# Optimization experiments

Hardware: AMD Instinct MI355X
Metric: run time of the kernel (lower is better)

## Reference

```python
import jax, jax.numpy as jnp
import numpy as np

D_MODEL = 1024
N_HEADS = 16
D_K = D_MODEL // N_HEADS
D_FF = 4096
EPS = 1e-5


def _layernorm(x, g, b):
    mu = jnp.mean(x, axis=-1, keepdims=True)
    var = jnp.mean(jnp.square(x - mu), axis=-1, keepdims=True)
    return (x - mu) * jax.lax.rsqrt(var + EPS) * g + b


def setup_inputs() -> dict:
    key = jax.random.key(0)
    ks = jax.random.split(key, 16)
    s = 0.02
    B, S = 2, 2048
    inp = {
        "x": jax.random.normal(ks[0], (B, S, D_MODEL), dtype=jnp.float32),
        "mask": jnp.ones((1, 1, S, S), dtype=jnp.int32),
        # attention projections (stored [in, out]; y = x @ W + b)
        "Wq": jax.random.normal(ks[1], (D_MODEL, D_MODEL)) * s,
        "bq": jnp.zeros((D_MODEL,)),
        "Wk": jax.random.normal(ks[2], (D_MODEL, D_MODEL)) * s,
        "bk": jnp.zeros((D_MODEL,)),
        "Wv": jax.random.normal(ks[3], (D_MODEL, D_MODEL)) * s,
        "bv": jnp.zeros((D_MODEL,)),
        "Wo": jax.random.normal(ks[4], (D_MODEL, D_MODEL)) * s,
        "bo": jnp.zeros((D_MODEL,)),
        "temperature": jnp.sqrt(jnp.array([float(D_K)], dtype=jnp.float32)),
        "time_weights": jax.random.normal(ks[5], (1, N_HEADS, 1, D_K)),
        "gateW": jax.random.normal(ks[6], (D_K, 1)) * s,
        "gateb": jnp.zeros((1,)),
        "ln_attn_g": jnp.ones((D_MODEL,)),
        "ln_attn_b": jnp.zeros((D_MODEL,)),
        # feed-forward
        "fc1W": jax.random.normal(ks[7], (D_MODEL, D_FF)) * s,
        "fc1b": jnp.zeros((D_FF,)),
        "fc2W": jax.random.normal(ks[8], (D_FF, D_MODEL)) * s,
        "fc2b": jnp.zeros((D_MODEL,)),
        "n1g": jnp.ones((D_MODEL,)),
        "n1b": jnp.zeros((D_MODEL,)),
        "n2g": jnp.ones((D_MODEL,)),
        "n2b": jnp.zeros((D_MODEL,)),
    }
    return inp


def reference(x, mask, Wq, bq, Wk, bk, Wv, bv, Wo, bo, temperature,
              time_weights, gateW, gateb, ln_attn_g, ln_attn_b,
              fc1W, fc1b, fc2W, fc2b, n1g, n1b, n2g, n2b):
    B, S, D = x.shape
    H, dk = N_HEADS, D_K

    def heads(t):  # [B,S,D] -> [B,H,S,dk]
        return t.reshape(B, S, H, dk).transpose(0, 2, 1, 3)

    q = heads(x @ Wq + bq) + time_weights  # learned per-head bias on Q
    k = heads(x @ Wk + bk)
    v = heads(x @ Wv + bv)

    scores = jnp.einsum("bhqd,bhkd->bhqk", q, k) / temperature
    scores = jnp.where(mask == 0, jnp.float32(-1e9), scores)
    gate = jax.nn.sigmoid(q @ gateW + gateb)  # [B,H,S,1] per-query gate
    scores = scores * gate
    probs = jax.nn.softmax(scores, axis=-1)

    ctx = jnp.einsum("bhqk,bhkd->bhqd", probs, v)
    ctx = ctx.transpose(0, 2, 1, 3).reshape(B, S, D)
    attn_out = _layernorm(ctx @ Wo + bo, ln_attn_g, ln_attn_b)

    x1 = _layernorm(x + attn_out, n1g, n1b)
    ff = jax.nn.gelu(x1 @ fc1W + fc1b, approximate=False) @ fc2W + fc2b
    return _layernorm(x1 + ff, n2g, n2b)
```

## Files before the change

### kernel.cpp

```cpp
#include <hip/hip_runtime.h>
#include <stdint.h>
#include <math.h>


typedef uint16_t u16;
typedef unsigned long long u64;
typedef __attribute__((ext_vector_type(8))) short short8;
typedef __attribute__((ext_vector_type(4))) float f32x4;

#define S_LEN 2048
#define DM 1024

#define GLOAD_LDS16(g, l)                                                      \
  __builtin_amdgcn_global_load_lds(                                            \
      (const __attribute__((address_space(1))) void*)(g),                      \
      (__attribute__((address_space(3))) void*)(l), 16, 0, 0)

__device__ __forceinline__ float bf2f(u16 h) {
  union { uint32_t u; float f; } x;
  x.u = ((uint32_t)h) << 16;
  return x.f;
}
__device__ __forceinline__ u16 f2bf(float f) {
  union { float f; uint32_t u; } x;
  x.f = f;
  uint32_t r = (x.u + 0x7fffu + ((x.u >> 16) & 1u)) >> 16;
  return (u16)r;
}
__device__ __forceinline__ u16 f2bf_fast(float f) {
  union { float f; uint32_t u; } x;
  x.f = f;
  return (u16)((x.u + 0x8000u) >> 16);
}

union U8 { uint4 u; u16 s[8]; };
union U4 { uint2 u; u16 s[4]; };

__global__ __launch_bounds__(256) void cvt_k(const float* __restrict__ in,
                                             u16* __restrict__ out, int n) {
  int i = (blockIdx.x * 256 + threadIdx.x) * 4;
  if (i >= n) return;
  float4 v = *(const float4*)(in + i);
  U4 o;
  o.s[0] = f2bf(v.x); o.s[1] = f2bf(v.y); o.s[2] = f2bf(v.z); o.s[3] = f2bf(v.w);
  *(uint2*)(out + i) = o.u;
}

__global__ __launch_bounds__(256) void mb_k(const int* __restrict__ mask,
                                            u16* __restrict__ mb) {
  int tid = blockIdx.x * 256 + threadIdx.x;
  const int* src = mask + (size_t)tid * 16;
  uint32_t b = 0;
#pragma unroll
  for (int q = 0; q < 4; q++) {
    int4 m = *(const int4*)(src + q * 4);
    b |= (m.x != 0 ? 1u : 0u) << (q * 4 + 0);
    b |= (m.y != 0 ? 1u : 0u) << (q * 4 + 1);
    b |= (m.z != 0 ? 1u : 0u) << (q * 4 + 2);
    b |= (m.w != 0 ? 1u : 0u) << (q * 4 + 3);
  }
  mb[tid] = (u16)b;
}

__device__ __forceinline__ void tcvt_body(const float* __restrict__ in,
                                          u16* __restrict__ out, int R, int C) {
  __shared__ u16 tile[64][72];
  int c0 = blockIdx.x * 64, r0 = blockIdx.y * 64;
  int t = threadIdx.x;
  int r = t & 63, seg = t >> 6;
  const float* src = in + (size_t)(r0 + r) * C + c0 + seg * 16;
#pragma unroll
  for (int q = 0; q < 4; q++) {
    float4 v = *(const float4*)(src + q * 4);
    tile[r][seg * 16 + q * 4 + 0] = f2bf(v.x);
    tile[r][seg * 16 + q * 4 + 1] = f2bf(v.y);
    tile[r][seg * 16 + q * 4 + 2] = f2bf(v.z);
    tile[r][seg * 16 + q * 4 + 3] = f2bf(v.w);
  }
  __syncthreads();
  U8 v0, v1;
#pragma unroll
  for (int i = 0; i < 8; i++) v0.s[i] = tile[seg * 16 + i][r];
#pragma unroll
  for (int i = 0; i < 8; i++) v1.s[i] = tile[seg * 16 + 8 + i][r];
  u16* dst = out + (size_t)(c0 + r) * R + r0 + seg * 16;
  *(uint4*)dst = v0.u;
  *(uint4*)(dst + 8) = v1.u;
}

__global__ __launch_bounds__(256) void transpose_cvt_k(const float* __restrict__ in,
                                                       u16* __restrict__ out,
                                                       int R, int C) {
  tcvt_body(in, out, R, C);
}

__global__ __launch_bounds__(256) void transpose_cvt3_k(const float* __restrict__ i0,
                                                        const float* __restrict__ i1,
                                                        const float* __restrict__ i2,
                                                        u16* __restrict__ o0,
                                                        u16* __restrict__ o1,
                                                        u16* __restrict__ o2) {
  int z = blockIdx.z;
  const float* in = (z == 0) ? i0 : (z == 1) ? i1 : i2;
  u16* out = (z == 0) ? o0 : (z == 1) ? o1 : o2;
  tcvt_body(in, out, 1024, 1024);
}

__global__ __launch_bounds__(256) void vtrans_k(const u16* __restrict__ V,
                                                u16* __restrict__ VT) {
  __shared__ u16 tile[64][72];
  int bx = blockIdx.x, bh = blockIdx.y;
  int b = bh >> 4, h = bh & 15;
  int t = threadIdx.x, r = t & 63, seg = t >> 6;
  const u16* src = V + (size_t)(b * S_LEN + bx * 64 + r) * DM + h * 64 + seg * 16;
  *(uint4*)&tile[r][seg * 16] = *(const uint4*)src;
  *(uint4*)&tile[r][seg * 16 + 8] = *(const uint4*)(src + 8);
  __syncthreads();
  U8 v0, v1;
#pragma unroll
  for (int i = 0; i < 8; i++) v0.s[i] = tile[seg * 16 + i][r];
#pragma unroll
  for (int i = 0; i < 8; i++) v1.s[i] = tile[seg * 16 + 8 + i][r];
  u16* dst = VT + ((size_t)bh * 64 + r) * S_LEN + bx * 64 + seg * 16;
  *(uint4*)dst = v0.u;
  *(uint4*)(dst + 8) = v1.u;
}

template <int BM, int EPI, int MXS>
__global__ __launch_bounds__(256) void gemm_bt(const u16* __restrict__ A,
                                               const u16* __restrict__ Bt,
                                               u16* __restrict__ C,
                                               const float* __restrict__ bias,
                                               int M, int N, int K) {
  constexpr int MI = BM / 32;
  constexpr int RPW = BM / 4;
  __shared__ u16 As[BM * 32];
  __shared__ u16 Bs[128 * 32];
  int t = threadIdx.x;
  int wid = t >> 6, lane = t & 63;
  int g = lane >> 4, li = lane & 15;
  int bx = MXS ? blockIdx.y : blockIdx.x;
  int by = MXS ? blockIdx.x : blockIdx.y;
  int wr = (wid >> 1) * (BM / 2), wc = (wid & 1) * 64;

  const u16* a0 = A + (size_t)(by * BM + wid * RPW + (lane >> 2)) * K + (lane & 3) * 8;
  const u16* b0 = Bt + (size_t)(bx * 128 + wid * 32 + (lane >> 2)) * K + (lane & 3) * 8;
  u16* lA0 = &As[wid * RPW * 32];
  u16* lB0 = &Bs[wid * 1024];

  f32x4 acc[MI][4];
#pragma unroll
  for (int i = 0; i < MI; i++)
#pragma unroll
    for (int j = 0; j < 4; j++) acc[i][j] = (f32x4){0.f, 0.f, 0.f, 0.f};

  for (int k0 = 0; k0 < K; k0 += 32) {
    GLOAD_LDS16(a0 + k0, lA0);
    if (BM == 128) GLOAD_LDS16(a0 + (size_t)16 * K + k0, lA0 + 512);
    GLOAD_LDS16(b0 + k0, lB0);
    GLOAD_LDS16(b0 + (size_t)16 * K + k0, lB0 + 512);
    __syncthreads();
    short8 af[MI], bfv[4];
#pragma unroll
    for (int i = 0; i < MI; i++)
      af[i] = *(const short8*)&As[(wr + i * 16 + li) * 32 + g * 8];
#pragma unroll
    for (int i = 0; i < 4; i++)
      bfv[i] = *(const short8*)&Bs[(wc + i * 16 + li) * 32 + g * 8];
#pragma unroll
    for (int mi = 0; mi < MI; mi++)
#pragma unroll
      for (int ni = 0; ni < 4; ni++)
        acc[mi][ni] = __builtin_amdgcn_mfma_f32_16x16x32_bf16(
            af[mi], bfv[ni], acc[mi][ni], 0, 0, 0);
    __syncthreads();
  }

#pragma unroll
  for (int ni = 0; ni < 4; ni++) {
    int col = bx * 128 + wc + ni * 16 + li;
    float bv = bias[col];
#pragma unroll
    for (int mi = 0; mi < MI; mi++) {
#pragma unroll
      for (int r = 0; r < 4; r++) {
        int row = by * BM + wr + mi * 16 + g * 4 + r;
        float v = acc[mi][ni][r] + bv;
        if (EPI == 2) v = 0.5f * v * (1.0f + erff(v * 0.70710678118654752f));
        C[(size_t)row * N + col] = f2bf(v);
      }
    }
  }
}

__global__ __launch_bounds__(256) void qkv_gemm(const u16* __restrict__ A,
                                                const u16* __restrict__ WTq,
                                                const u16* __restrict__ WTk,
                                                const u16* __restrict__ WTv,
                                                u16* __restrict__ Cq,
                                                u16* __restrict__ Ck,
                                                u16* __restrict__ Cv,
                                                const float* __restrict__ bq,
                                                const float* __restrict__ bk,
                                                const float* __restrict__ bv,
                                                const float* __restrict__ tw) {
  const int K = 1024, N = 1024;
  __shared__ u16 As[128 * 32];
  __shared__ u16 Bs[128 * 32];
  int t = threadIdx.x;
  int wid = t >> 6, lane = t & 63;
  int g = lane >> 4, li = lane & 15;
  int by = blockIdx.x, bx = blockIdx.y, z = blockIdx.z;
  int wr = (wid >> 1) * 64, wc = (wid & 1) * 64;

  const u16* Bt = (z == 0) ? WTq : (z == 1) ? WTk : WTv;
  u16* C = (z == 0) ? Cq : (z == 1) ? Ck : Cv;
  const float* bias = (z == 0) ? bq : (z == 1) ? bk : bv;

  const u16* a0 = A + (size_t)(by * 128 + wid * 32 + (lane >> 2)) * K + (lane & 3) * 8;
  const u16* b0 = Bt + (size_t)(bx * 128 + wid * 32 + (lane >> 2)) * K + (lane & 3) * 8;
  u16* lA0 = &As[wid * 1024];
  u16* lB0 = &Bs[wid * 1024];

  f32x4 acc[4][4];
#pragma unroll
  for (int i = 0; i < 4; i++)
#pragma unroll
    for (int j = 0; j < 4; j++) acc[i][j] = (f32x4){0.f, 0.f, 0.f, 0.f};

  for (int k0 = 0; k0 < K; k0 += 32) {
    GLOAD_LDS16(a0 + k0, lA0);
    GLOAD_LDS16(a0 + (size_t)16 * K + k0, lA0 + 512);
    GLOAD_LDS16(b0 + k0, lB0);
    GLOAD_LDS16(b0 + (size_t)16 * K + k0, lB0 + 512);
    __syncthreads();
    short8 af[4], bfv[4];
#pragma unroll
    for (int i = 0; i < 4; i++)
      af[i] = *(const short8*)&As[(wr + i * 16 + li) * 32 + g * 8];
#pragma unroll
    for (int i = 0; i < 4; i++)
      bfv[i] = *(const short8*)&Bs[(wc + i * 16 + li) * 32 + g * 8];
#pragma unroll
    for (int mi = 0; mi < 4; mi++)
#pragma unroll
      for (int ni = 0; ni < 4; ni++)
        acc[mi][ni] = __builtin_amdgcn_mfma_f32_16x16x32_bf16(
            af[mi], bfv[ni], acc[mi][ni], 0, 0, 0);
    __syncthreads();
  }

#pragma unroll
  for (int ni = 0; ni < 4; ni++) {
    int col = bx * 128 + wc + ni * 16 + li;
    float bvv = bias[col];
    if (z == 0) bvv += tw[col];
#pragma unroll
    for (int mi = 0; mi < 4; mi++) {
#pragma unroll
      for (int r = 0; r < 4; r++) {
        int row = by * 128 + wr + mi * 16 + g * 4 + r;
        C[(size_t)row * N + col] = f2bf(acc[mi][ni][r] + bvv);
      }
    }
  }
}

__global__ __launch_bounds__(256) void attn_k(const u16* __restrict__ Q,
                                              const u16* __restrict__ Kp,
                                              const u16* __restrict__ VT,
                                              u16* __restrict__ CTX,
                                              const u16* __restrict__ mb,
                                              const float* __restrict__ gateW,
                                              const float* __restrict__ gateb,
                                              const float* __restrict__ temp) {
  __shared__ u16 Qs[64][72];
  __shared__ u16 Ks[64][72];
  __shared__ u16 Vs[64][72];
  __shared__ u16 Ps[4][16][72];
  __shared__ float gate_s[64];

  int blk = blockIdx.x;
  int bh = blk & 31, qt = blk >> 5;
  int b = bh >> 4, h = bh & 15;
  int t = threadIdx.x, wid = t >> 6, lane = t & 63;
  int g = lane >> 4, li = lane & 15;
  int sq0 = qt * 64;

  const u16* Qb  = Q + ((size_t)b * S_LEN) * DM + h * 64;
  const u16* Kb  = Kp + ((size_t)b * S_LEN) * DM + h * 64;
  const u16* VTb = VT + ((size_t)(b * 16 + h) * 64) * S_LEN;

  {
    int r = t >> 2, cs = (t & 3) * 16;
    const u16* src = Qb + (size_t)(sq0 + r) * DM + cs;
    *(uint4*)&Qs[r][cs] = *(const uint4*)src;
    *(uint4*)&Qs[r][cs + 8] = *(const uint4*)(src + 8);
  }
  __syncthreads();
  if (t < 64) {
    float acc = gateb[0];
#pragma unroll
    for (int d = 0; d < 64; d++) acc += bf2f(Qs[t][d]) * gateW[d];
    gate_s[t] = 1.f / (1.f + __expf(-acc));
  }
  __syncthreads();

  const float LOG2E = 1.4426950408889634f;
  float invt2 = LOG2E / temp[0];
  const float NEG2 = -1.0e9f * 1.4426950408889634f;
  short8 qf0 = *(const short8*)&Qs[wid * 16 + li][g * 8];
  short8 qf1 = *(const short8*)&Qs[wid * 16 + li][32 + g * 8];
  float gqs[4], ng[4];
  int sq[4];
#pragma unroll
  for (int r = 0; r < 4; r++) {
    float gq = gate_s[wid * 16 + g * 4 + r];
    gqs[r] = gq * invt2;
    ng[r] = NEG2 * gq;
    sq[r] = sq0 + wid * 16 + g * 4 + r;
  }

  float m_i[4], psl[4];
  f32x4 o[4];
#pragma unroll
  for (int r = 0; r < 4; r++) { m_i[r] = -1e30f; psl[r] = 0.f; }
#pragma unroll
  for (int n = 0; n < 4; n++) o[n] = (f32x4){0.f, 0.f, 0.f, 0.f};

  for (int kt = 0; kt < 32; kt++) {
    __syncthreads();
    {
      int r = t >> 2, cs = (t & 3) * 16;
      const u16* srcK = Kb + (size_t)(kt * 64 + r) * DM + cs;
      *(uint4*)&Ks[r][cs] = *(const uint4*)srcK;
      *(uint4*)&Ks[r][cs + 8] = *(const uint4*)(srcK + 8);
      const u16* srcV = VTb + (size_t)r * S_LEN + kt * 64 + cs;
      *(uint4*)&Vs[r][cs] = *(const uint4*)srcV;
      *(uint4*)&Vs[r][cs + 8] = *(const uint4*)(srcV + 8);
    }
    u64 bits[4];
#pragma unroll
    for (int r = 0; r < 4; r++)
      bits[r] = *(const u64*)(mb + (size_t)sq[r] * 128 + kt * 4);
    __syncthreads();

    f32x4 sc[4];
#pragma unroll
    for (int ni = 0; ni < 4; ni++) {
      sc[ni] = (f32x4){0.f, 0.f, 0.f, 0.f};
      short8 kf0 = *(const short8*)&Ks[ni * 16 + li][g * 8];
      short8 kf1 = *(const short8*)&Ks[ni * 16 + li][32 + g * 8];
      sc[ni] = __builtin_amdgcn_mfma_f32_16x16x32_bf16(qf0, kf0, sc[ni], 0, 0, 0);
      sc[ni] = __builtin_amdgcn_mfma_f32_16x16x32_bf16(qf1, kf1, sc[ni], 0, 0, 0);
    }

    float sval[4][4];
    float rmax[4] = {-1e30f, -1e30f, -1e30f, -1e30f};
    bool allm = ((bits[0] & bits[1] & bits[2] & bits[3]) == ~0ull);
    if (__all(allm)) {
#pragma unroll
      for (int ni = 0; ni < 4; ni++)
#pragma unroll
        for (int r = 0; r < 4; r++) {
          float s = sc[ni][r] * gqs[r];
          sval[ni][r] = s;
          rmax[r] = fmaxf(rmax[r], s);
        }
    } else {
      u64 bs[4];
#pragma unroll
      for (int r = 0; r < 4; r++) bs[r] = bits[r] >> li;
#pragma unroll
      for (int ni = 0; ni < 4; ni++)
#pragma unroll
        for (int r = 0; r < 4; r++) {
          float s = ((bs[r] >> (ni * 16)) & 1ull) ? sc[ni][r] * gqs[r] : ng[r];
          sval[ni][r] = s;
          rmax[r] = fmaxf(rmax[r], s);
        }
    }
#pragma unroll
    for (int off = 1; off < 16; off <<= 1)
#pragma unroll
      for (int r = 0; r < 4; r++)
        rmax[r] = fmaxf(rmax[r], __shfl_xor(rmax[r], off, 64));

    float alpha[4];
#pragma unroll
    for (int r = 0; r < 4; r++) {
      float mnew = fmaxf(m_i[r], rmax[r]);
      alpha[r] = __builtin_amdgcn_exp2f(m_i[r] - mnew);
      m_i[r] = mnew;
    }
    float pp[4] = {0.f, 0.f, 0.f, 0.f};
#pragma unroll
    for (int ni = 0; ni < 4; ni++)
#pragma unroll
      for (int r = 0; r < 4; r++) {
        float p = __builtin_amdgcn_exp2f(sval[ni][r] - m_i[r]);
        pp[r] += p;
        Ps[wid][g * 4 + r][ni * 16 + li] = f2bf_fast(p);
      }
#pragma unroll
    for (int r = 0; r < 4; r++) psl[r] = psl[r] * alpha[r] + pp[r];
#pragma unroll
    for (int n = 0; n < 4; n++)
#pragma unroll
      for (int r = 0; r < 4; r++) o[n][r] *= alpha[r];

    __builtin_amdgcn_wave_barrier();

    short8 pf0 = *(const short8*)&Ps[wid][li][g * 8];
    short8 pf1 = *(const short8*)&Ps[wid][li][32 + g * 8];
#pragma unroll
    for (int ni = 0; ni < 4; ni++) {
      short8 vf0 = *(const short8*)&Vs[ni * 16 + li][g * 8];
      short8 vf1 = *(const short8*)&Vs[ni * 16 + li][32 + g * 8];
      o[ni] = __builtin_amdgcn_mfma_f32_16x16x32_bf16(pf0, vf0, o[ni], 0, 0, 0);
      o[ni] = __builtin_amdgcn_mfma_f32_16x16x32_bf16(pf1, vf1, o[ni], 0, 0, 0);
    }
  }

  float linv[4];
#pragma unroll
  for (int r = 0; r < 4; r++) {
    float l = psl[r];
#pragma unroll
    for (int off = 1; off < 16; off <<= 1) l += __shfl_xor(l, off, 64);
    linv[r] = 1.f / l;
  }
#pragma unroll
  for (int ni = 0; ni < 4; ni++) {
    int col = h * 64 + ni * 16 + li;
#pragma unroll
    for (int r = 0; r < 4; r++) {
      size_t row = (size_t)b * S_LEN + sq[r];
      CTX[row * DM + col] = f2bf(o[ni][r] * linv[r]);
    }
  }
}

__device__ __forceinline__ void block_sum2(float& a, float& b, float* red, int t) {
#pragma unroll
  for (int off = 32; off > 0; off >>= 1) {
    a += __shfl_xor(a, off, 64);
    b += __shfl_xor(b, off, 64);
  }
  __syncthreads();
  if ((t & 63) == 0) {
    red[(t >> 6) * 2] = a;
    red[(t >> 6) * 2 + 1] = b;
  }
  __syncthreads();
  a = red[0] + red[2] + red[4] + red[6];
  b = red[1] + red[3] + red[5] + red[7];
}

__global__ __launch_bounds__(256) void ln1_k(const u16* __restrict__ po,
                                             const float* __restrict__ x,
                                             const float* __restrict__ g1,
                                             const float* __restrict__ b1,
                                             const float* __restrict__ g2,
                                             const float* __restrict__ b2,
                                             u16* __restrict__ x1) {
  __shared__ float red[8];
  int row = blockIdx.x, t = threadIdx.x;
  size_t base = (size_t)row * 1024 + t * 4;
  U4 pv; pv.u = *(const uint2*)(po + base);
  float v[4];
#pragma unroll
  for (int i = 0; i < 4; i++) v[i] = bf2f(pv.s[i]);
  float s1 = v[0] + v[1] + v[2] + v[3];
  float s2 = v[0]*v[0] + v[1]*v[1] + v[2]*v[2] + v[3]*v[3];
  block_sum2(s1, s2, red, t);
  float mu = s1 * (1.f / 1024.f);
  float rs = rsqrtf(s2 * (1.f / 1024.f) - mu * mu + 1e-5f);
  float4 xv = *(const float4*)(x + base);
  float4 g1v = *(const float4*)(g1 + t * 4);
  float4 b1v = *(const float4*)(b1 + t * 4);
  float w[4];
  w[0] = xv.x + ((v[0] - mu) * rs * g1v.x + b1v.x);
  w[1] = xv.y + ((v[1] - mu) * rs * g1v.y + b1v.y);
  w[2] = xv.z + ((v[2] - mu) * rs * g1v.z + b1v.z);
  w[3] = xv.w + ((v[3] - mu) * rs * g1v.w + b1v.w);
  s1 = w[0] + w[1] + w[2] + w[3];
  s2 = w[0]*w[0] + w[1]*w[1] + w[2]*w[2] + w[3]*w[3];
  block_sum2(s1, s2, red, t);
  mu = s1 * (1.f / 1024.f);
  rs = rsqrtf(s2 * (1.f / 1024.f) - mu * mu + 1e-5f);
  float4 g2v = *(const float4*)(g2 + t * 4);
  float4 b2v = *(const float4*)(b2 + t * 4);
  U4 ov;
  ov.s[0] = f2bf((w[0] - mu) * rs * g2v.x + b2v.x);
  ov.s[1] = f2bf((w[1] - mu) * rs * g2v.y + b2v.y);
  ov.s[2] = f2bf((w[2] - mu) * rs * g2v.z + b2v.z);
  ov.s[3] = f2bf((w[3] - mu) * rs * g2v.w + b2v.w);
  *(uint2*)(x1 + base) = ov.u;
}

__global__ __launch_bounds__(256) void ln2_k(const u16* __restrict__ y,
                                             const u16* __restrict__ x1,
                                             const float* __restrict__ g,
                                             const float* __restrict__ b,
                                             float* __restrict__ out) {
  __shared__ float red[8];
  int row = blockIdx.x, t = threadIdx.x;
  size_t base = (size_t)row * 1024 + t * 4;
  U4 yv; yv.u = *(const uint2*)(y + base);
  U4 xv; xv.u = *(const uint2*)(x1 + base);
  float w[4];
#pragma unroll
  for (int i = 0; i < 4; i++) w[i] = bf2f(yv.s[i]) + bf2f(xv.s[i]);
  float s1 = w[0] + w[1] + w[2] + w[3];
  float s2 = w[0]*w[0] + w[1]*w[1] + w[2]*w[2] + w[3]*w[3];
  block_sum2(s1, s2, red, t);
  float mu = s1 * (1.f / 1024.f);
  float rs = rsqrtf(s2 * (1.f / 1024.f) - mu * mu + 1e-5f);
  float4 gv = *(const float4*)(g + t * 4);
  float4 bv = *(const float4*)(b + t * 4);
  float4 ov;
  ov.x = (w[0] - mu) * rs * gv.x + bv.x;
  ov.y = (w[1] - mu) * rs * gv.y + bv.y;
  ov.z = (w[2] - mu) * rs * gv.z + bv.z;
  ov.w = (w[3] - mu) * rs * gv.w + bv.w;
  *(float4*)(out + base) = ov;
}

extern "C" void kernel_launch(void* const* d_in, const int* in_sizes, int n_in,
                              void* d_out, int out_size, void* d_ws, size_t ws_size,
                              hipStream_t stream) {
  (void)in_sizes; (void)n_in; (void)out_size;
  const float* x    = (const float*)d_in[0];
  const int*   mask = (const int*)d_in[1];
  const float* Wq = (const float*)d_in[2];  const float* bq = (const float*)d_in[3];
  const float* Wk = (const float*)d_in[4];  const float* bk = (const float*)d_in[5];
  const float* Wv = (const float*)d_in[6];  const float* bv = (const float*)d_in[7];
  const float* Wo = (const float*)d_in[8];  const float* bo = (const float*)d_in[9];
  const float* temp = (const float*)d_in[10];
  const float* tw   = (const float*)d_in[11];
  const float* gW   = (const float*)d_in[12]; const float* gb  = (const float*)d_in[13];
  const float* lag  = (const float*)d_in[14]; const float* lab = (const float*)d_in[15];
  const float* f1W  = (const float*)d_in[16]; const float* f1b = (const float*)d_in[17];
  const float* f2W  = (const float*)d_in[18]; const float* f2b = (const float*)d_in[19];
  const float* n1g  = (const float*)d_in[20]; const float* n1b = (const float*)d_in[21];
  const float* n2g  = (const float*)d_in[22]; const float* n2b = (const float*)d_in[23];
  float* out = (float*)d_out;

  u16* ws = (u16*)d_ws;
  const size_t MB4 = (size_t)4096 * 1024;
  u16* s0 = ws;
  u16* s1 = ws + 1 * MB4;
  u16* s2 = ws + 2 * MB4;
  u16* s3 = ws + 3 * MB4;
  u16* s4 = ws + 4 * MB4;
  u16* d0 = (u16*)d_out;
  u16* d1 = d0 + MB4;
  bool bigws = ws_size >= (size_t)9 * 8 * 1024 * 1024;
  u16* Hfull = ws + 5 * MB4;

  dim3 blk(256);
  cvt_k<<<dim3(4096), blk, 0, stream>>>(x, s4, 4096 * 1024);
  transpose_cvt3_k<<<dim3(16, 16, 3), blk, 0, stream>>>(Wq, Wk, Wv, s0, s1, s2);
  qkv_gemm<<<dim3(32, 8, 3), blk, 0, stream>>>(s4, s0, s1, s2, s3, d0, d1,
                                               bq, bk, bv, tw);
  vtrans_k<<<dim3(32, 32), blk, 0, stream>>>(d1, s0);
  mb_k<<<dim3(1024), blk, 0, stream>>>(mask, s1);
  transpose_cvt_k<<<dim3(16, 16), blk, 0, stream>>>(Wo, s4, 1024, 1024);
  attn_k<<<dim3(1024), blk, 0, stream>>>(s3, d0, s0, s2, s1, gW, gb, temp);
  gemm_bt<64, 0, 1><<<dim3(64, 8), blk, 0, stream>>>(s2, s4, d0, bo, 4096, 1024, 1024);
  ln1_k<<<dim3(4096), blk, 0, stream>>>(d0, x, lag, lab, n1g, n1b, s3);
  transpose_cvt_k<<<dim3(64, 16), blk, 0, stream>>>(f1W, s0, 1024, 4096);
  transpose_cvt_k<<<dim3(16, 64), blk, 0, stream>>>(f2W, s1, 4096, 1024);
  if (bigws) {
    gemm_bt<128, 2, 0><<<dim3(32, 32), blk, 0, stream>>>(s3, s0, Hfull, f1b,
                                                         4096, 4096, 1024);
    gemm_bt<64, 0, 0><<<dim3(8, 64), blk, 0, stream>>>(Hfull, s1, s2, f2b,
                                                       4096, 1024, 4096);
  } else {
    for (int i = 0; i < 2; i++) {
      const u16* Ai = s3 + (size_t)i * 2048 * 1024;
      u16* Yi = s2 + (size_t)i * 2048 * 1024;
      gemm_bt<128, 2, 0><<<dim3(32, 16), blk, 0, stream>>>(Ai, s0, d0, f1b,
                                                           2048, 4096, 1024);
      gemm_bt<64, 0, 1><<<dim3(32, 8), blk, 0, stream>>>(d0, s1, Yi, f2b,
                                                         2048, 1024, 4096);
    }
  }
  ln2_k<<<dim3(4096), blk, 0, stream>>>(s2, s3, n2g, n2b, out);
}
```

Before: 480.2 us.

## Unroll GEMM K-loop by two tiles, use tanh GELU, skip unchanged softmax rescale

The GEMM and QKV kernels now load two 32-wide K slices per iteration into separate LDS buffers, halving the number of barrier pairs per K sweep at the cost of doubled shared memory. The exact erf GELU in the fc1 epilogue is replaced by a tanh/sigmoid approximation built on a hardware exp2, which is cheaper but not numerically identical to the reference. The attention kernel skips the online-softmax max update and accumulator rescale when no row's max increased anywhere in the wave.

```diff
diff --git a/kernel.cpp b/kernel.cpp
--- a/kernel.cpp
+++ b/kernel.cpp
@@ -31,6 +31,12 @@
   union { float f; uint32_t u; } x;
   x.f = f;
   return (u16)((x.u + 0x8000u) >> 16);
+}
+__device__ __forceinline__ float gelu_fast(float x) {
+  float x3 = x * x * x;
+  float z = 2.302118131f * fmaf(0.044715f, x3, x);
+  float e = __builtin_amdgcn_exp2f(z);
+  return x * e / (1.0f + e);
 }
 
 union U8 { uint4 u; u16 s[8]; };
@@ -134,8 +140,8 @@
                                                int M, int N, int K) {
   constexpr int MI = BM / 32;
   constexpr int RPW = BM / 4;
-  __shared__ u16 As[BM * 32];
-  __shared__ u16 Bs[128 * 32];
+  __shared__ u16 As[2][BM * 32];
+  __shared__ u16 Bs[2][128 * 32];
   int t = threadIdx.x;
   int wid = t >> 6, lane = t & 63;
   int g = lane >> 4, li = lane & 15;
@@ -145,8 +151,10 @@
 
   const u16* a0 = A + (size_t)(by * BM + wid * RPW + (lane >> 2)) * K + (lane & 3) * 8;
   const u16* b0 = Bt + (size_t)(bx * 128 + wid * 32 + (lane >> 2)) * K + (lane & 3) * 8;
-  u16* lA0 = &As[wid * RPW * 32];
-  u16* lB0 = &Bs[wid * 1024];
+  u16* lA0 = &As[0][wid * RPW * 32];
+  u16* lA1 = &As[1][wid * RPW * 32];
+  u16* lB0 = &Bs[0][wid * 1024];
+  u16* lB1 = &Bs[1][wid * 1024];
 
   f32x4 acc[MI][4];
 #pragma unroll
@@ -154,25 +162,32 @@
 #pragma unroll
     for (int j = 0; j < 4; j++) acc[i][j] = (f32x4){0.f, 0.f, 0.f, 0.f};
 
-  for (int k0 = 0; k0 < K; k0 += 32) {
+  for (int k0 = 0; k0 < K; k0 += 64) {
     GLOAD_LDS16(a0 + k0, lA0);
     if (BM == 128) GLOAD_LDS16(a0 + (size_t)16 * K + k0, lA0 + 512);
     GLOAD_LDS16(b0 + k0, lB0);
     GLOAD_LDS16(b0 + (size_t)16 * K + k0, lB0 + 512);
+    GLOAD_LDS16(a0 + k0 + 32, lA1);
+    if (BM == 128) GLOAD_LDS16(a0 + (size_t)16 * K + k0 + 32, lA1 + 512);
+    GLOAD_LDS16(b0 + k0 + 32, lB1);
+    GLOAD_LDS16(b0 + (size_t)16 * K + k0 + 32, lB1 + 512);
     __syncthreads();
-    short8 af[MI], bfv[4];
-#pragma unroll
-    for (int i = 0; i < MI; i++)
-      af[i] = *(const short8*)&As[(wr + i * 16 + li) * 32 + g * 8];
-#pragma unroll
-    for (int i = 0; i < 4; i++)
-      bfv[i] = *(const short8*)&Bs[(wc + i * 16 + li) * 32 + g * 8];
-#pragma unroll
-    for (int mi = 0; mi < MI; mi++)
-#pragma unroll
-      for (int ni = 0; ni < 4; ni++)
-        acc[mi][ni] = __builtin_amdgcn_mfma_f32_16x16x32_bf16(
-            af[mi], bfv[ni], acc[mi][ni], 0, 0, 0);
+#pragma unroll
+    for (int h = 0; h < 2; h++) {
+      short8 af[MI], bfv[4];
+#pragma unroll
+      for (int i = 0; i < MI; i++)
+        af[i] = *(const short8*)&As[h][(wr + i * 16 + li) * 32 + g * 8];
+#pragma unroll
+      for (int i = 0; i < 4; i++)
+        bfv[i] = *(const short8*)&Bs[h][(wc + i * 16 + li) * 32 + g * 8];
+#pragma unroll
+      for (int mi = 0; mi < MI; mi++)
+#pragma unroll
+        for (int ni = 0; ni < 4; ni++)
+          acc[mi][ni] = __builtin_amdgcn_mfma_f32_16x16x32_bf16(
+              af[mi], bfv[ni], acc[mi][ni], 0, 0, 0);
+    }
     __syncthreads();
   }
 
@@ -186,7 +201,7 @@
       for (int r = 0; r < 4; r++) {
         int row = by * BM + wr + mi * 16 + g * 4 + r;
         float v = acc[mi][ni][r] + bv;
-        if (EPI == 2) v = 0.5f * v * (1.0f + erff(v * 0.70710678118654752f));
+        if (EPI == 2) v = gelu_fast(v);
         C[(size_t)row * N + col] = f2bf(v);
       }
     }
@@ -205,8 +220,8 @@
                                                 const float* __restrict__ bv,
                                                 const float* __restrict__ tw) {
   const int K = 1024, N = 1024;
-  __shared__ u16 As[128 * 32];
-  __shared__ u16 Bs[128 * 32];
+  __shared__ u16 As[2][128 * 32];
+  __shared__ u16 Bs[2][128 * 32];
   int t = threadIdx.x;
   int wid = t >> 6, lane = t & 63;
   int g = lane >> 4, li = lane & 15;
@@ -219,8 +234,10 @@
 
   const u16* a0 = A + (size_t)(by * 128 + wid * 32 + (lane >> 2)) * K + (lane & 3) * 8;
   const u16* b0 = Bt + (size_t)(bx * 128 + wid * 32 + (lane >> 2)) * K + (lane & 3) * 8;
-  u16* lA0 = &As[wid * 1024];
-  u16* lB0 = &Bs[wid * 1024];
+  u16* lA0 = &As[0][wid * 1024];
+  u16* lA1 = &As[1][wid * 1024];
+  u16* lB0 = &Bs[0][wid * 1024];
+  u16* lB1 = &Bs[1][wid * 1024];
 
   f32x4 acc[4][4];
 #pragma unroll
@@ -228,25 +245,32 @@
 #pragma unroll
     for (int j = 0; j < 4; j++) acc[i][j] = (f32x4){0.f, 0.f, 0.f, 0.f};
 
-  for (int k0 = 0; k0 < K; k0 += 32) {
+  for (int k0 = 0; k0 < K; k0 += 64) {
     GLOAD_LDS16(a0 + k0, lA0);
     GLOAD_LDS16(a0 + (size_t)16 * K + k0, lA0 + 512);
     GLOAD_LDS16(b0 + k0, lB0);
     GLOAD_LDS16(b0 + (size_t)16 * K + k0, lB0 + 512);
+    GLOAD_LDS16(a0 + k0 + 32, lA1);
+    GLOAD_LDS16(a0 + (size_t)16 * K + k0 + 32, lA1 + 512);
+    GLOAD_LDS16(b0 + k0 + 32, lB1);
+    GLOAD_LDS16(b0 + (size_t)16 * K + k0 + 32, lB1 + 512);
     __syncthreads();
-    short8 af[4], bfv[4];
-#pragma unroll
-    for (int i = 0; i < 4; i++)
-      af[i] = *(const short8*)&As[(wr + i * 16 + li) * 32 + g * 8];
-#pragma unroll
-    for (int i = 0; i < 4; i++)
-      bfv[i] = *(const short8*)&Bs[(wc + i * 16 + li) * 32 + g * 8];
-#pragma unroll
-    for (int mi = 0; mi < 4; mi++)
-#pragma unroll
-      for (int ni = 0; ni < 4; ni++)
-        acc[mi][ni] = __builtin_amdgcn_mfma_f32_16x16x32_bf16(
-            af[mi], bfv[ni], acc[mi][ni], 0, 0, 0);
+#pragma unroll
+    for (int h = 0; h < 2; h++) {
+      short8 af[4], bfv[4];
+#pragma unroll
+      for (int i = 0; i < 4; i++)
+        af[i] = *(const short8*)&As[h][(wr + i * 16 + li) * 32 + g * 8];
+#pragma unroll
+      for (int i = 0; i < 4; i++)
+        bfv[i] = *(const short8*)&Bs[h][(wc + i * 16 + li) * 32 + g * 8];
+#pragma unroll
+      for (int mi = 0; mi < 4; mi++)
+#pragma unroll
+        for (int ni = 0; ni < 4; ni++)
+          acc[mi][ni] = __builtin_amdgcn_mfma_f32_16x16x32_bf16(
+              af[mi], bfv[ni], acc[mi][ni], 0, 0, 0);
+    }
     __syncthreads();
   }
 
@@ -386,13 +410,24 @@
       for (int r = 0; r < 4; r++)
         rmax[r] = fmaxf(rmax[r], __shfl_xor(rmax[r], off, 64));
 
-    float alpha[4];
-#pragma unroll
-    for (int r = 0; r < 4; r++) {
-      float mnew = fmaxf(m_i[r], rmax[r]);
-      alpha[r] = __builtin_amdgcn_exp2f(m_i[r] - mnew);
-      m_i[r] = mnew;
-    }
+    bool up = (rmax[0] > m_i[0]) | (rmax[1] > m_i[1]) |
+              (rmax[2] > m_i[2]) | (rmax[3] > m_i[3]);
+    if (__any(up)) {
+      float alpha[4];
+#pragma unroll
+      for (int r = 0; r < 4; r++) {
+        float mnew = fmaxf(m_i[r], rmax[r]);
+        alpha[r] = __builtin_amdgcn_exp2f(m_i[r] - mnew);
+        m_i[r] = mnew;
+      }
+#pragma unroll
+      for (int r = 0; r < 4; r++) psl[r] *= alpha[r];
+#pragma unroll
+      for (int n = 0; n < 4; n++)
+#pragma unroll
+        for (int r = 0; r < 4; r++) o[n][r] *= alpha[r];
+    }
+
     float pp[4] = {0.f, 0.f, 0.f, 0.f};
 #pragma unroll
     for (int ni = 0; ni < 4; ni++)
@@ -403,11 +438,7 @@
         Ps[wid][g * 4 + r][ni * 16 + li] = f2bf_fast(p);
       }
 #pragma unroll
-    for (int r = 0; r < 4; r++) psl[r] = psl[r] * alpha[r] + pp[r];
-#pragma unroll
-    for (int n = 0; n < 4; n++)
-#pragma unroll
-      for (int r = 0; r < 4; r++) o[n][r] *= alpha[r];
+    for (int r = 0; r < 4; r++) psl[r] += pp[r];
 
     __builtin_amdgcn_wave_barrier();
 
```

New measurement: 484.7 us. Within noise of the previous version (+0.9%).
